# Kernel optimization log

Measured on AMD Instinct MI355X. Metric: run time of the kernel, lower is better.

## Reference

```python
import jax, jax.numpy as jnp
import numpy as np

B, S, D = 4, 2048, 2048
H = 16
Q_LORA = 1536
KV_LORA = 512
D_NOPE = 128
D_ROPE = 64
D_V = 128
MLP = 8192
EPS = 1e-6
THETA = 10000.0


def rmsnorm(x, scale, eps=EPS):
    var = jnp.mean(jnp.square(x.astype(jnp.float32)), axis=-1, keepdims=True)
    return (x * jax.lax.rsqrt(var + eps)).astype(x.dtype) * scale


def rope(x, positions):
    # x: [B, S, H, d], positions: [B, S]
    d = x.shape[-1]
    inv_freq = 1.0 / (THETA ** (jnp.arange(0, d, 2, dtype=jnp.float32) / d))
    ang = positions.astype(jnp.float32)[..., None] * inv_freq  # [B,S,d/2]
    cos = jnp.cos(ang)[:, :, None, :]
    sin = jnp.sin(ang)[:, :, None, :]
    x1, x2 = jnp.split(x, 2, axis=-1)
    return jnp.concatenate([x1 * cos - x2 * sin, x2 * cos + x1 * sin], axis=-1)


def setup_inputs() -> dict:
    key = jax.random.key(0)
    ks = jax.random.split(key, 16)
    sd = lambda fan: 1.0 / np.sqrt(fan)
    inp = {
        'inputs': jax.random.normal(ks[0], (B, S, D), jnp.float32),
        'decoder_segment_ids': jnp.ones((B, S), jnp.int32),
        'decoder_positions': jnp.broadcast_to(jnp.arange(S, dtype=jnp.int32), (B, S)),
        'pre_ln_scale': jnp.ones((D,), jnp.float32),
        'post_ln_scale': jnp.ones((D,), jnp.float32),
        'q_ln_scale': jnp.ones((Q_LORA,), jnp.float32),
        'kv_ln_scale': jnp.ones((KV_LORA,), jnp.float32),
        'wq_a': jax.random.normal(ks[1], (D, Q_LORA), jnp.float32) * sd(D),
        'wq_b': jax.random.normal(ks[2], (Q_LORA, H, D_NOPE + D_ROPE), jnp.float32) * sd(Q_LORA),
        'wkv_a': jax.random.normal(ks[3], (D, KV_LORA + D_ROPE), jnp.float32) * sd(D),
        'wkv_b': jax.random.normal(ks[4], (KV_LORA, H, D_NOPE + D_V), jnp.float32) * sd(KV_LORA),
        'wo_attn': jax.random.normal(ks[5], (H, D_V, D), jnp.float32) * sd(H * D_V),
        'wi_0': jax.random.normal(ks[6], (D, MLP), jnp.float32) * sd(D),
        'wi_1': jax.random.normal(ks[7], (D, MLP), jnp.float32) * sd(D),
        'wo_mlp': jax.random.normal(ks[8], (MLP, D), jnp.float32) * sd(MLP),
    }
    return inp


def reference(inputs, decoder_segment_ids, decoder_positions, pre_ln_scale, post_ln_scale,
              q_ln_scale, kv_ln_scale, wq_a, wq_b, wkv_a, wkv_b, wo_attn, wi_0, wi_1, wo_mlp):
    # ---- pre-norm ----
    lnx = rmsnorm(inputs, pre_ln_scale)

    # ---- MLA attention ----
    # low-rank query: down-proj, norm, up-proj
    q_c = rmsnorm(lnx @ wq_a, q_ln_scale)                       # [B,S,Q_LORA]
    q = jnp.einsum('bsr,rhd->bshd', q_c, wq_b)                  # [B,S,H,nope+rope]
    q_nope, q_rope = q[..., :D_NOPE], q[..., D_NOPE:]

    # compressed kv + decoupled rope key
    kv = lnx @ wkv_a                                            # [B,S,KV_LORA+rope]
    c_kv = rmsnorm(kv[..., :KV_LORA], kv_ln_scale)
    k_rope = kv[..., KV_LORA:][:, :, None, :]                   # [B,S,1,rope]
    kvu = jnp.einsum('bsr,rhd->bshd', c_kv, wkv_b)              # [B,S,H,nope+v]
    k_nope, v = kvu[..., :D_NOPE], kvu[..., D_NOPE:]

    q_rope = rope(q_rope, decoder_positions)
    k_rope = rope(k_rope, decoder_positions)
    k_rope = jnp.broadcast_to(k_rope, (B, S, H, D_ROPE))

    qf = jnp.concatenate([q_nope, q_rope], axis=-1)             # [B,S,H,192]
    kf = jnp.concatenate([k_nope, k_rope], axis=-1)

    scale = 1.0 / np.sqrt(D_NOPE + D_ROPE)
    scores = jnp.einsum('bqhd,bkhd->bhqk', qf, kf) * scale      # [B,H,S,S]

    pos = decoder_positions
    seg = decoder_segment_ids
    mask = (pos[:, :, None] >= pos[:, None, :]) & (seg[:, :, None] == seg[:, None, :])
    scores = jnp.where(mask[:, None, :, :], scores, -1e9)
    probs = jax.nn.softmax(scores, axis=-1)

    attn = jnp.einsum('bhqk,bkhd->bqhd', probs, v)              # [B,S,H,D_V]
    attn_out = jnp.einsum('bqhd,hdm->bqm', attn, wo_attn)       # [B,S,D]

    # ---- residual + post-norm ----
    intermediate = inputs + attn_out
    hidden = rmsnorm(intermediate, post_ln_scale)

    # ---- gated MLP (silu * linear) ----
    mlp = (jax.nn.silu(hidden @ wi_0) * (hidden @ wi_1)) @ wo_mlp

    return mlp + intermediate
```

## Files before the change

### kernel.cpp

```cpp
#include <hip/hip_runtime.h>
#include <stdint.h>

typedef unsigned short u16;
typedef __bf16 bf16x8 __attribute__((ext_vector_type(8)));
typedef float f32x4 __attribute__((ext_vector_type(4)));

#define B_ 4
#define S_ 2048
#define H_ 16
#define TOK (B_*S_)
#define MFMA_B16 __builtin_amdgcn_mfma_f32_16x16x32_bf16
#define LGKM0 asm volatile("s_waitcnt lgkmcnt(0)" ::: "memory")
#define VMC(n) asm volatile("s_waitcnt vmcnt(" #n ")" ::: "memory")
#define SB0 __builtin_amdgcn_sched_barrier(0)

__device__ __forceinline__ u16 f32_bf16(float f) {
    union { float f; unsigned int u; } x; x.f = f;
    return (u16)((x.u + 0x7fffu + ((x.u >> 16) & 1u)) >> 16);
}
__device__ __forceinline__ float bf2f(u16 v) {
    union { unsigned int u; float f; } x; x.u = ((unsigned int)v) << 16; return x.f;
}
__device__ __forceinline__ void gld_lds16(const u16* g, u16* lds) {
    __builtin_amdgcn_global_load_lds(
        (const __attribute__((address_space(1))) unsigned int*)g,
        (__attribute__((address_space(3))) unsigned int*)lds, 16, 0, 0);
}

__global__ void fill_sentinel(float* o, int n) {
    int i = blockIdx.x * 256 + threadIdx.x;
    if (i < n) o[i] = 12345.0f;
}

__global__ __launch_bounds__(256) void transpose_f32_bf16(const float* __restrict__ in, u16* __restrict__ out,
                                                          int K, int N, int Npad) {
    __shared__ float t[32][33];
    int nb = blockIdx.x * 32, kb = blockIdx.y * 32;
    int c = threadIdx.x & 31, r = threadIdx.x >> 5;
#pragma unroll
    for (int i = 0; i < 4; ++i) {
        int kk = kb + r + i * 8, nn = nb + c;
        t[r + i * 8][c] = (kk < K && nn < N) ? in[(size_t)kk * N + nn] : 0.f;
    }
    __syncthreads();
#pragma unroll
    for (int i = 0; i < 4; ++i) {
        int no = nb + r + i * 8, ko = kb + c;
        if (no < Npad && ko < K) out[(size_t)no * K + ko] = f32_bf16(t[c][r + i * 8]);
    }
}

__global__ __launch_bounds__(256) void rmsnorm_f32(const float* __restrict__ in, const float* __restrict__ sc,
                                                   u16* __restrict__ out, int N) {
    int row = blockIdx.x;
    const float* x = in + (size_t)row * N;
    float ss = 0.f;
    for (int c = threadIdx.x * 4; c < N; c += 1024) {
        float4 v = *(const float4*)(x + c);
        ss += v.x * v.x + v.y * v.y + v.z * v.z + v.w * v.w;
    }
#pragma unroll
    for (int off = 32; off; off >>= 1) ss += __shfl_down(ss, off);
    __shared__ float red[4];
    if ((threadIdx.x & 63) == 0) red[threadIdx.x >> 6] = ss;
    __syncthreads();
    float rs = rsqrtf((red[0] + red[1] + red[2] + red[3]) / (float)N + 1e-6f);
    for (int c = threadIdx.x * 4; c < N; c += 1024) {
        float4 v = *(const float4*)(x + c);
        float4 s4 = *(const float4*)(sc + c);
        ushort4 ov;
        ov.x = f32_bf16(v.x * rs * s4.x);
        ov.y = f32_bf16(v.y * rs * s4.y);
        ov.z = f32_bf16(v.z * rs * s4.z);
        ov.w = f32_bf16(v.w * rs * s4.w);
        *(ushort4*)&out[(size_t)row * N + c] = ov;
    }
}

__global__ __launch_bounds__(256) void rmsnorm_bf16(const u16* __restrict__ in, const float* __restrict__ sc,
                                                    u16* __restrict__ out, int N) {
    int row = blockIdx.x;
    const u16* x = in + (size_t)row * N;
    float ss = 0.f;
    for (int c = threadIdx.x * 8; c < N; c += 2048) {
        ushort4 v0 = *(const ushort4*)(x + c);
        ushort4 v1 = *(const ushort4*)(x + c + 4);
        float f0 = bf2f(v0.x), f1 = bf2f(v0.y), f2 = bf2f(v0.z), f3 = bf2f(v0.w);
        float f4 = bf2f(v1.x), f5 = bf2f(v1.y), f6 = bf2f(v1.z), f7 = bf2f(v1.w);
        ss += f0*f0 + f1*f1 + f2*f2 + f3*f3 + f4*f4 + f5*f5 + f6*f6 + f7*f7;
    }
#pragma unroll
    for (int off = 32; off; off >>= 1) ss += __shfl_down(ss, off);
    __shared__ float red[4];
    if ((threadIdx.x & 63) == 0) red[threadIdx.x >> 6] = ss;
    __syncthreads();
    float rs = rsqrtf((red[0] + red[1] + red[2] + red[3]) / (float)N + 1e-6f);
    for (int c = threadIdx.x * 8; c < N; c += 2048) {
        ushort4 v0 = *(const ushort4*)(x + c);
        ushort4 v1 = *(const ushort4*)(x + c + 4);
        ushort4 o0, o1;
        o0.x = f32_bf16(bf2f(v0.x) * rs * sc[c + 0]);
        o0.y = f32_bf16(bf2f(v0.y) * rs * sc[c + 1]);
        o0.z = f32_bf16(bf2f(v0.z) * rs * sc[c + 2]);
        o0.w = f32_bf16(bf2f(v0.w) * rs * sc[c + 3]);
        o1.x = f32_bf16(bf2f(v1.x) * rs * sc[c + 4]);
        o1.y = f32_bf16(bf2f(v1.y) * rs * sc[c + 5]);
        o1.z = f32_bf16(bf2f(v1.z) * rs * sc[c + 6]);
        o1.w = f32_bf16(bf2f(v1.w) * rs * sc[c + 7]);
        *(ushort4*)&out[(size_t)row * N + c] = o0;
        *(ushort4*)&out[(size_t)row * N + c + 4] = o1;
    }
}

__global__ __launch_bounds__(128) void kv_post(const u16* __restrict__ kv, const float* __restrict__ scale,
                                               const int* __restrict__ pos, u16* __restrict__ ckv,
                                               u16* __restrict__ kr) {
    int row = blockIdx.x;
    const u16* x = kv + (size_t)row * 640;
    int c = threadIdx.x * 4;
    ushort4 v = *(const ushort4*)(x + c);
    float f0 = bf2f(v.x), f1 = bf2f(v.y), f2 = bf2f(v.z), f3 = bf2f(v.w);
    float ss = f0*f0 + f1*f1 + f2*f2 + f3*f3;
#pragma unroll
    for (int off = 32; off; off >>= 1) ss += __shfl_down(ss, off);
    __shared__ float red[2];
    if ((threadIdx.x & 63) == 0) red[threadIdx.x >> 6] = ss;
    __syncthreads();
    float rs = rsqrtf((red[0] + red[1]) * (1.f / 512.f) + 1e-6f);
    float4 s4 = *(const float4*)(scale + c);
    ushort4 ov;
    ov.x = f32_bf16(f0 * rs * s4.x);
    ov.y = f32_bf16(f1 * rs * s4.y);
    ov.z = f32_bf16(f2 * rs * s4.z);
    ov.w = f32_bf16(f3 * rs * s4.w);
    *(ushort4*)&ckv[(size_t)row * 512 + c] = ov;
    if (threadIdx.x < 32) {
        int i = threadIdx.x;
        float x1 = bf2f(x[512 + i]), x2 = bf2f(x[544 + i]);
        float inv = expf(-(float)(2 * i) * (1.f / 64.f) * 9.2103403719761836f);
        float ang = (float)pos[row] * inv;
        float sn, cs; sincosf(ang, &sn, &cs);
        kr[(size_t)row * 64 + i]      = f32_bf16(x1 * cs - x2 * sn);
        kr[(size_t)row * 64 + 32 + i] = f32_bf16(x2 * cs + x1 * sn);
    }
}

__global__ __launch_bounds__(64) void q_rope_inplace(u16* __restrict__ q, const int* __restrict__ pos) {
    int token = blockIdx.x, h = blockIdx.y;
    u16* p = q + ((size_t)token * 16 + h) * 192;
    int t = threadIdx.x, i = t & 31;
    float x1 = bf2f(p[128 + i]), x2 = bf2f(p[160 + i]);
    float inv = expf(-(float)(2 * i) * (1.f / 64.f) * 9.2103403719761836f);
    float ang = (float)pos[token] * inv;
    float sn, cs; sincosf(ang, &sn, &cs);
    float val = (t < 32) ? (x1 * cs - x2 * sn) : (x2 * cs + x1 * sn);
    p[128 + t] = f32_bf16(val);
}

__global__ __launch_bounds__(320) void kv_build(const u16* __restrict__ kvu, const u16* __restrict__ kr,
                                                u16* __restrict__ kf, u16* __restrict__ vf, int tok0) {
    int local = blockIdx.x, h = blockIdx.y;
    int token = tok0 + local;
    int b = token >> 11, s = token & 2047;
    int bh = b * 16 + h;
    int tile = s >> 6, ki = s & 63;
    const u16* u = kvu + ((size_t)local * 16 + h) * 256;
    int t = threadIdx.x;
    if (t < 192) {
        u16 val = (t < 128) ? u[t] : kr[(size_t)token * 64 + (t - 128)];
        int byte = (ki * 384 + t * 2) ^ ((ki & 7) << 4);
        kf[(size_t)bh * (S_ * 192) + (size_t)tile * 12288 + (byte >> 1)] = val;
    } else {
        int dv = t - 192;
        u16 val = u[128 + dv];
        int byte = (dv * 128 + ki * 2) ^ ((dv & 7) << 4);
        vf[(size_t)bh * (S_ * 128) + (size_t)tile * 8192 + (byte >> 1)] = val;
    }
}

__global__ __launch_bounds__(256) void gemm128(const u16* __restrict__ A, const u16* __restrict__ Bt,
                                               u16* __restrict__ C, int M, int N, int K) {
    __shared__ u16 As[128 * 32];
    __shared__ u16 Bs[128 * 32];
    const int l = threadIdx.x & 63, w = threadIdx.x >> 6;
    const int wr = w >> 1, wc = w & 1;
    const int m0 = blockIdx.y * 128, n0 = blockIdx.x * 128;
    const int lm = l & 15, lg = l >> 4;
    const int srow = l >> 2, sk = (l & 3) * 8;
    f32x4 acc[4][4] = {};
    for (int k0 = 0; k0 < K; k0 += 32) {
#pragma unroll
        for (int i = 0; i < 2; ++i) {
            int c = w * 2 + i;
            gld_lds16(A  + (size_t)(m0 + c * 16 + srow) * K + k0 + sk, &As[c * 512]);
            gld_lds16(Bt + (size_t)(n0 + c * 16 + srow) * K + k0 + sk, &Bs[c * 512]);
        }
        __syncthreads();
        bf16x8 a[4], b[4];
#pragma unroll
        for (int m = 0; m < 4; ++m) a[m] = *(const bf16x8*)&As[(wr * 64 + m * 16 + lm) * 32 + lg * 8];
#pragma unroll
        for (int n = 0; n < 4; ++n) b[n] = *(const bf16x8*)&Bs[(wc * 64 + n * 16 + lm) * 32 + lg * 8];
#pragma unroll
        for (int m = 0; m < 4; ++m)
#pragma unroll
            for (int n = 0; n < 4; ++n)
                acc[m][n] = MFMA_B16(a[m], b[n], acc[m][n], 0, 0, 0);
        __syncthreads();
    }
#pragma unroll
    for (int m = 0; m < 4; ++m)
#pragma unroll
        for (int j = 0; j < 4; ++j) {
            int row = m0 + wr * 64 + m * 16 + lg * 4 + j;
            size_t base = (size_t)row * N + n0 + wc * 64;
#pragma unroll
            for (int n = 0; n < 4; ++n)
                C[base + n * 16 + lm] = f32_bf16(acc[m][n][j]);
        }
}

template<int EPI>
__global__ __launch_bounds__(512, 1) void gemm256(const u16* __restrict__ A, const u16* __restrict__ Bt,
                                                  void* __restrict__ Cv, const void* __restrict__ Rv,
                                                  int M, int N, int K) {
    __shared__ u16 lds[65536];
    char* ldsb = (char*)lds;
    const int tid = threadIdx.x;
    const int l = tid & 63, w = tid >> 6;
    const int wr = w >> 2, wcn = w & 3;
    const int lm = l & 15, lg = l >> 4;
    const int m0 = blockIdx.y * 256, n0 = blockIdx.x * 256;

    int sr[2], scb[2];
#pragma unroll
    for (int ld = 0; ld < 2; ++ld) {
        int P = tid * 16 + ld * 8192;
        sr[ld] = P >> 7;
        scb[ld] = (P & 127) ^ ((sr[ld] & 7) << 4);
    }
    const u16* Ab = A + (size_t)m0 * K;
    const u16* Bb = Bt + (size_t)n0 * K;

    f32x4 acc[8][4] = {};

    auto stageU = [&](int unit, int tt) {
#pragma unroll
        for (int ld = 0; ld < 2; ++ld) {
            int r = sr[ld];
            const u16* src;
            if (unit == 0)      src = Ab + (size_t)((r >> 6) * 128 + (r & 63)) * K + tt * 64 + (scb[ld] >> 1);
            else if (unit == 1) src = Ab + (size_t)((r >> 6) * 128 + 64 + (r & 63)) * K + tt * 64 + (scb[ld] >> 1);
            else if (unit == 2) src = Bb + (size_t)((r >> 5) * 64 + (r & 31)) * K + tt * 64 + (scb[ld] >> 1);
            else                src = Bb + (size_t)((r >> 5) * 64 + 32 + (r & 31)) * K + tt * 64 + (scb[ld] >> 1);
            gld_lds16(src, (u16*)(ldsb + (tt & 1) * 65536 + unit * 16384 + tid * 16 + ld * 8192));
        }
    };
    auto readA = [&](int buf, int fm, int ks) -> bf16x8 {
        int lr = wr * 64 + (fm & 3) * 16 + lm;
        int byte = lr * 128 + ((ks * 64 + lg * 16) ^ ((lr & 7) << 4));
        return *(const bf16x8*)(ldsb + buf * 65536 + (fm >> 2) * 16384 + byte);
    };
    auto readB = [&](int buf, int fn, int ks) -> bf16x8 {
        int lr = wcn * 32 + (fn & 1) * 16 + lm;
        int byte = lr * 128 + ((ks * 64 + lg * 16) ^ ((lr & 7) << 4));
        return *(const bf16x8*)(ldsb + buf * 65536 + (2 + (fn >> 1)) * 16384 + byte);
    };

    const int nt = K >> 6;
    stageU(0, 0); stageU(2, 0); stageU(3, 0); stageU(1, 0);
    VMC(2);
    __builtin_amdgcn_s_barrier();

#pragma unroll 1
    for (int t = 0; t < nt; ++t) {
        const int buf = t & 1;
        const bool nx = (t + 1 < nt);
        bf16x8 a0, a1, a2, a3, a4, a5, a6, a7;
        bf16x8 b0 = readB(buf, 0, 0), b1 = readB(buf, 0, 1), b2 = readB(buf, 1, 0), b3 = readB(buf, 1, 1);
        a0 = readA(buf, 0, 0); a1 = readA(buf, 0, 1); a2 = readA(buf, 1, 0); a3 = readA(buf, 1, 1);
        a4 = readA(buf, 2, 0); a5 = readA(buf, 2, 1); a6 = readA(buf, 3, 0); a7 = readA(buf, 3, 1);
        if (nx) stageU(0, t + 1);
        __builtin_amdgcn_s_barrier();
        LGKM0;
        SB0;
        __builtin_amdgcn_s_setprio(1);
        acc[0][0] = MFMA_B16(a0, b0, acc[0][0], 0, 0, 0);
        acc[0][0] = MFMA_B16(a1, b1, acc[0][0], 0, 0, 0);
        acc[0][1] = MFMA_B16(a0, b2, acc[0][1], 0, 0, 0);
        acc[0][1] = MFMA_B16(a1, b3, acc[0][1], 0, 0, 0);
        acc[1][0] = MFMA_B16(a2, b0, acc[1][0], 0, 0, 0);
        acc[1][0] = MFMA_B16(a3, b1, acc[1][0], 0, 0, 0);
        acc[1][1] = MFMA_B16(a2, b2, acc[1][1], 0, 0, 0);
        acc[1][1] = MFMA_B16(a3, b3, acc[1][1], 0, 0, 0);
        acc[2][0] = MFMA_B16(a4, b0, acc[2][0], 0, 0, 0);
        acc[2][0] = MFMA_B16(a5, b1, acc[2][0], 0, 0, 0);
        acc[2][1] = MFMA_B16(a4, b2, acc[2][1], 0, 0, 0);
        acc[2][1] = MFMA_B16(a5, b3, acc[2][1], 0, 0, 0);
        acc[3][0] = MFMA_B16(a6, b0, acc[3][0], 0, 0, 0);
        acc[3][0] = MFMA_B16(a7, b1, acc[3][0], 0, 0, 0);
        acc[3][1] = MFMA_B16(a6, b2, acc[3][1], 0, 0, 0);
        acc[3][1] = MFMA_B16(a7, b3, acc[3][1], 0, 0, 0);
        __builtin_amdgcn_s_setprio(0);
        __builtin_amdgcn_s_barrier();
        bf16x8 c0 = readB(buf, 2, 0), c1 = readB(buf, 2, 1), c2 = readB(buf, 3, 0), c3 = readB(buf, 3, 1);
        if (nx) { stageU(2, t + 1); VMC(4); } else { VMC(0); }
        __builtin_amdgcn_s_barrier();
        LGKM0;
        SB0;
        __builtin_amdgcn_s_setprio(1);
        acc[0][2] = MFMA_B16(a0, c0, acc[0][2], 0, 0, 0);
        acc[0][2] = MFMA_B16(a1, c1, acc[0][2], 0, 0, 0);
        acc[0][3] = MFMA_B16(a0, c2, acc[0][3], 0, 0, 0);
        acc[0][3] = MFMA_B16(a1, c3, acc[0][3], 0, 0, 0);
        acc[1][2] = MFMA_B16(a2, c0, acc[1][2], 0, 0, 0);
        acc[1][2] = MFMA_B16(a3, c1, acc[1][2], 0, 0, 0);
        acc[1][3] = MFMA_B16(a2, c2, acc[1][3], 0, 0, 0);
        acc[1][3] = MFMA_B16(a3, c3, acc[1][3], 0, 0, 0);
        acc[2][2] = MFMA_B16(a4, c0, acc[2][2], 0, 0, 0);
        acc[2][2] = MFMA_B16(a5, c1, acc[2][2], 0, 0, 0);
        acc[2][3] = MFMA_B16(a4, c2, acc[2][3], 0, 0, 0);
        acc[2][3] = MFMA_B16(a5, c3, acc[2][3], 0, 0, 0);
        acc[3][2] = MFMA_B16(a6, c0, acc[3][2], 0, 0, 0);
        acc[3][2] = MFMA_B16(a7, c1, acc[3][2], 0, 0, 0);
        acc[3][3] = MFMA_B16(a6, c2, acc[3][3], 0, 0, 0);
        acc[3][3] = MFMA_B16(a7, c3, acc[3][3], 0, 0, 0);
        __builtin_amdgcn_s_setprio(0);
        __builtin_amdgcn_s_barrier();
        a0 = readA(buf, 4, 0); a1 = readA(buf, 4, 1); a2 = readA(buf, 5, 0); a3 = readA(buf, 5, 1);
        a4 = readA(buf, 6, 0); a5 = readA(buf, 6, 1); a6 = readA(buf, 7, 0); a7 = readA(buf, 7, 1);
        if (nx) stageU(3, t + 1);
        __builtin_amdgcn_s_barrier();
        LGKM0;
        SB0;
        __builtin_amdgcn_s_setprio(1);
        acc[4][2] = MFMA_B16(a0, c0, acc[4][2], 0, 0, 0);
        acc[4][2] = MFMA_B16(a1, c1, acc[4][2], 0, 0, 0);
        acc[4][3] = MFMA_B16(a0, c2, acc[4][3], 0, 0, 0);
        acc[4][3] = MFMA_B16(a1, c3, acc[4][3], 0, 0, 0);
        acc[5][2] = MFMA_B16(a2, c0, acc[5][2], 0, 0, 0);
        acc[5][2] = MFMA_B16(a3, c1, acc[5][2], 0, 0, 0);
        acc[5][3] = MFMA_B16(a2, c2, acc[5][3], 0, 0, 0);
        acc[5][3] = MFMA_B16(a3, c3, acc[5][3], 0, 0, 0);
        acc[6][2] = MFMA_B16(a4, c0, acc[6][2], 0, 0, 0);
        acc[6][2] = MFMA_B16(a5, c1, acc[6][2], 0, 0, 0);
        acc[6][3] = MFMA_B16(a4, c2, acc[6][3], 0, 0, 0);
        acc[6][3] = MFMA_B16(a5, c3, acc[6][3], 0, 0, 0);
        acc[7][2] = MFMA_B16(a6, c0, acc[7][2], 0, 0, 0);
        acc[7][2] = MFMA_B16(a7, c1, acc[7][2], 0, 0, 0);
        acc[7][3] = MFMA_B16(a6, c2, acc[7][3], 0, 0, 0);
        acc[7][3] = MFMA_B16(a7, c3, acc[7][3], 0, 0, 0);
        __builtin_amdgcn_s_setprio(0);
        __builtin_amdgcn_s_barrier();
        if (nx) { stageU(1, t + 1); VMC(2); }
        __builtin_amdgcn_s_barrier();
        SB0;
        __builtin_amdgcn_s_setprio(1);
        acc[4][0] = MFMA_B16(a0, b0, acc[4][0], 0, 0, 0);
        acc[4][0] = MFMA_B16(a1, b1, acc[4][0], 0, 0, 0);
        acc[4][1] = MFMA_B16(a0, b2, acc[4][1], 0, 0, 0);
        acc[4][1] = MFMA_B16(a1, b3, acc[4][1], 0, 0, 0);
        acc[5][0] = MFMA_B16(a2, b0, acc[5][0], 0, 0, 0);
        acc[5][0] = MFMA_B16(a3, b1, acc[5][0], 0, 0, 0);
        acc[5][1] = MFMA_B16(a2, b2, acc[5][1], 0, 0, 0);
        acc[5][1] = MFMA_B16(a3, b3, acc[5][1], 0, 0, 0);
        acc[6][0] = MFMA_B16(a4, b0, acc[6][0], 0, 0, 0);
        acc[6][0] = MFMA_B16(a5, b1, acc[6][0], 0, 0, 0);
        acc[6][1] = MFMA_B16(a4, b2, acc[6][1], 0, 0, 0);
        acc[6][1] = MFMA_B16(a5, b3, acc[6][1], 0, 0, 0);
        acc[7][0] = MFMA_B16(a6, b0, acc[7][0], 0, 0, 0);
        acc[7][0] = MFMA_B16(a7, b1, acc[7][0], 0, 0, 0);
        acc[7][1] = MFMA_B16(a6, b2, acc[7][1], 0, 0, 0);
        acc[7][1] = MFMA_B16(a7, b3, acc[7][1], 0, 0, 0);
        __builtin_amdgcn_s_setprio(0);
        __builtin_amdgcn_s_barrier();
    }
#pragma unroll
    for (int fm = 0; fm < 8; ++fm)
#pragma unroll
        for (int j = 0; j < 4; ++j) {
            int row = m0 + wr * 128 + fm * 16 + lg * 4 + j;
            size_t base = (size_t)row * N + n0 + wcn * 64;
#pragma unroll
            for (int fn = 0; fn < 4; ++fn) {
                size_t idx = base + fn * 16 + lm;
                float v = acc[fm][fn][j];
                if (EPI == 0) {
                    ((u16*)Cv)[idx] = f32_bf16(v);
                } else if (EPI == 1) {
                    ((float*)Cv)[idx] = v + ((const float*)Rv)[idx];
                } else {
                    float x0 = bf2f(((const u16*)Rv)[idx]);
                    float sl = x0 / (1.f + expf(-x0));
                    ((u16*)Cv)[idx] = f32_bf16(sl * v);
                }
            }
        }
}

__global__ __launch_bounds__(256, 3) void attn_fwd(const u16* __restrict__ qf, const u16* __restrict__ kfs,
                                                   const u16* __restrict__ vfs, u16* __restrict__ attn) {
    __shared__ u16 Ks[64 * 192];
    __shared__ u16 Vs[128 * 64];
    __shared__ u16 Ps[4][1024];
    const int lin = blockIdx.y * gridDim.x + blockIdx.x;
    const int xcd = lin & 7, j = lin >> 3;
    const int bh = xcd * 8 + (j >> 4);
    const int px = j & 15;
    const int b = bh >> 4, h = bh & 15;
    const int l = threadIdx.x & 63, w = threadIdx.x >> 6;
    const int lm = l & 15, g = l >> 4;
    const u16* kb0 = kfs + (size_t)bh * (S_ * 192);
    const u16* vb0 = vfs + (size_t)bh * (S_ * 128);
    const float scale = 0.07216878364870322f;

    auto stageK = [&](int kt2) {
        const u16* kc = kb0 + (size_t)kt2 * 12288;
#pragma unroll
        for (int i = 0; i < 6; ++i) {
            int c = w + i * 4;
            gld_lds16(kc + c * 512 + l * 8, &Ks[c * 512]);
        }
    };
    auto stageV = [&](int kt2) {
        const u16* vc = vb0 + (size_t)kt2 * 8192;
#pragma unroll
        for (int i = 0; i < 4; ++i) {
            int c = w + i * 4;
            gld_lds16(vc + c * 512 + l * 8, &Vs[c * 512]);
        }
    };

    stageK(0);

    for (int pass = 0; pass < 2; ++pass) {
        const int qb = pass ? (31 - px) : px;
        const int qrow = qb * 64 + w * 16 + lm;
        const u16* qp = qf + (((size_t)(b * S_ + qrow)) * 16 + h) * 192 + g * 8;
        bf16x8 qr[6];
#pragma unroll
        for (int c = 0; c < 6; ++c) qr[c] = *(const bf16x8*)(qp + c * 32);
        f32x4 o[8] = {};
        float mrow[4] = {-1e30f, -1e30f, -1e30f, -1e30f};
        float lrow[4] = {0.f, 0.f, 0.f, 0.f};
        for (int kt = 0; kt <= qb; ++kt) {
            __syncthreads();
            stageV(kt);
            f32x4 sc[4] = {};
#pragma unroll
            for (int nf = 0; nf < 4; ++nf) {
                int key = nf * 16 + lm;
                int kswz = (key & 7) << 4;
#pragma unroll
                for (int c = 0; c < 6; ++c) {
                    int byte = (key * 384 + (c * 32 + g * 8) * 2) ^ kswz;
                    bf16x8 kv = *(const bf16x8*)((const char*)Ks + byte);
                    sc[nf] = MFMA_B16(qr[c], kv, sc[nf], 0, 0, 0);
                }
            }
            LGKM0;
            __builtin_amdgcn_s_barrier();
            if (kt < qb) stageK(kt + 1);
#pragma unroll
            for (int jj = 0; jj < 4; ++jj) {
                const int q_g = qb * 64 + w * 16 + g * 4 + jj;
                float mx = -1e30f;
#pragma unroll
                for (int nf = 0; nf < 4; ++nf) {
                    int key_g = kt * 64 + nf * 16 + lm;
                    float v = sc[nf][jj] * scale;
                    v = (key_g > q_g) ? -1e30f : v;
                    sc[nf][jj] = v;
                    mx = fmaxf(mx, v);
                }
                mx = fmaxf(mx, __shfl_xor(mx, 1));
                mx = fmaxf(mx, __shfl_xor(mx, 2));
                mx = fmaxf(mx, __shfl_xor(mx, 4));
                mx = fmaxf(mx, __shfl_xor(mx, 8));
                float newm = fmaxf(mrow[jj], mx);
                float fac = __expf(mrow[jj] - newm);
                mrow[jj] = newm;
                float rs = 0.f;
                u16 pb[4];
#pragma unroll
                for (int nf = 0; nf < 4; ++nf) {
                    float pv = __expf(sc[nf][jj] - newm);
                    rs += pv;
                    pb[nf] = f32_bf16(pv);
                }
                rs += __shfl_xor(rs, 1);
                rs += __shfl_xor(rs, 2);
                rs += __shfl_xor(rs, 4);
                rs += __shfl_xor(rs, 8);
                lrow[jj] = lrow[jj] * fac + rs;
#pragma unroll
                for (int n = 0; n < 8; ++n) o[n][jj] *= fac;
                int row = g * 4 + jj;
                int rswz = (row & 7) << 4;
#pragma unroll
                for (int nf = 0; nf < 4; ++nf) {
                    int byte = (row * 128 + (nf * 16 + lm) * 2) ^ rswz;
                    *(u16*)((char*)&Ps[w][0] + byte) = pb[nf];
                }
            }
            if (kt < qb) { VMC(6); } else { VMC(0); }
            __builtin_amdgcn_s_barrier();
            SB0;
#pragma unroll
            for (int kc2 = 0; kc2 < 2; ++kc2) {
                int pbyte = (lm * 128 + (kc2 * 32 + g * 8) * 2) ^ ((lm & 7) << 4);
                bf16x8 pa = *(const bf16x8*)((const char*)&Ps[w][0] + pbyte);
#pragma unroll
                for (int n = 0; n < 8; ++n) {
                    int dv = n * 16 + lm;
                    int vbyte = (dv * 128 + (kc2 * 32 + g * 8) * 2) ^ ((dv & 7) << 4);
                    bf16x8 vv = *(const bf16x8*)((const char*)Vs + vbyte);
                    o[n] = MFMA_B16(pa, vv, o[n], 0, 0, 0);
                }
            }
        }
#pragma unroll
        for (int jj = 0; jj < 4; ++jj) {
            float inv = 1.f / lrow[jj];
            int s = qb * 64 + w * 16 + g * 4 + jj;
            size_t base = ((size_t)(b * S_ + s)) * (H_ * 128) + h * 128;
#pragma unroll
            for (int n = 0; n < 8; ++n)
                attn[base + n * 16 + lm] = f32_bf16(o[n][jj] * inv);
        }
        if (pass == 0) stageK(0);
    }
}

extern "C" void kernel_launch(void* const* d_in, const int* in_sizes, int n_in,
                              void* d_out, int out_size, void* d_ws, size_t ws_size,
                              hipStream_t stream) {
    (void)in_sizes; (void)n_in;
    const float* inputs = (const float*)d_in[0];
    const int*   pos    = (const int*)d_in[2];
    const float* pre_s  = (const float*)d_in[3];
    const float* post_s = (const float*)d_in[4];
    const float* q_s    = (const float*)d_in[5];
    const float* kv_s   = (const float*)d_in[6];
    const float* wq_a   = (const float*)d_in[7];
    const float* wq_b   = (const float*)d_in[8];
    const float* wkv_a  = (const float*)d_in[9];
    const float* wkv_b  = (const float*)d_in[10];
    const float* wo_at  = (const float*)d_in[11];
    const float* wi0    = (const float*)d_in[12];
    const float* wi1    = (const float*)d_in[13];
    const float* wom    = (const float*)d_in[14];
    float* out = (float*)d_out;

    char* p = (char*)d_ws;
    auto alloc = [&](size_t n) { char* r = p; p += (n + 255) & ~(size_t)255; return r; };
    char* R1   = alloc((size_t)134217728);
    u16* vf    = (u16*)alloc((size_t)33554432);
    u16* aslot = (u16*)alloc((size_t)33554432);
    u16* wslot = (u16*)alloc((size_t)33554432);
    u16* ckv   = (u16*)alloc((size_t)8388608);
    u16* krope = (u16*)alloc((size_t)1048576);
    if ((size_t)(p - (char*)d_ws) > ws_size) {
        fill_sentinel<<<(out_size + 255) / 256, 256, 0, stream>>>(out, out_size);
        return;
    }
    u16* kf    = (u16*)R1;
    u16* q_c   = (u16*)R1;
    u16* kvtmp = (u16*)(R1 + 25165824);
    u16* q     = (u16*)(R1 + 50331648);
    u16* lnx   = (u16*)(R1 + 100663296);
    u16* kvu   = (u16*)(R1 + 100663296);
    u16* X     = (u16*)R1;

    rmsnorm_f32<<<TOK, 256, 0, stream>>>(inputs, pre_s, lnx, 2048);
    transpose_f32_bf16<<<dim3(48, 64), 256, 0, stream>>>(wq_a, wslot, 2048, 1536, 1536);
    gemm256<0><<<dim3(6, 32), 512, 0, stream>>>(lnx, wslot, q_c, nullptr, TOK, 1536, 2048);
    rmsnorm_bf16<<<TOK, 256, 0, stream>>>(q_c, q_s, q_c, 1536);
    transpose_f32_bf16<<<dim3(20, 64), 256, 0, stream>>>(wkv_a, wslot, 2048, 576, 640);
    gemm128<<<dim3(5, 64), 256, 0, stream>>>(lnx, wslot, kvtmp, TOK, 640, 2048);
    kv_post<<<TOK, 128, 0, stream>>>(kvtmp, kv_s, pos, ckv, krope);
    transpose_f32_bf16<<<dim3(96, 48), 256, 0, stream>>>(wq_b, wslot, 1536, 3072, 3072);
    gemm256<0><<<dim3(12, 32), 512, 0, stream>>>(q_c, wslot, q, nullptr, TOK, 3072, 1536);
    q_rope_inplace<<<dim3(TOK, 16), 64, 0, stream>>>(q, pos);
    transpose_f32_bf16<<<dim3(128, 16), 256, 0, stream>>>(wkv_b, wslot, 512, 4096, 4096);
    for (int ch = 0; ch < 2; ++ch) {
        int t0 = ch * 4096;
        gemm256<0><<<dim3(16, 16), 512, 0, stream>>>(ckv + (size_t)t0 * 512, wslot, kvu, nullptr, 4096, 4096, 512);
        kv_build<<<dim3(4096, 16), 320, 0, stream>>>(kvu, krope, kf, vf, t0);
    }
    attn_fwd<<<dim3(16, 64), 256, 0, stream>>>(q, kf, vf, aslot);
    transpose_f32_bf16<<<dim3(64, 64), 256, 0, stream>>>(wo_at, wslot, 2048, 2048, 2048);
    gemm256<1><<<dim3(8, 32), 512, 0, stream>>>(aslot, wslot, out, inputs, TOK, 2048, 2048);
    rmsnorm_f32<<<TOK, 256, 0, stream>>>(out, post_s, aslot, 2048);
    transpose_f32_bf16<<<dim3(256, 64), 256, 0, stream>>>(wi0, wslot, 2048, 8192, 8192);
    gemm256<0><<<dim3(32, 32), 512, 0, stream>>>(aslot, wslot, X, nullptr, TOK, 8192, 2048);
    transpose_f32_bf16<<<dim3(256, 64), 256, 0, stream>>>(wi1, wslot, 2048, 8192, 8192);
    gemm256<2><<<dim3(32, 32), 512, 0, stream>>>(aslot, wslot, X, X, TOK, 8192, 2048);
    transpose_f32_bf16<<<dim3(64, 256), 256, 0, stream>>>(wom, wslot, 8192, 2048, 2048);
    gemm256<1><<<dim3(8, 32), 512, 0, stream>>>(X, wslot, out, out, TOK, 2048, 8192);
}
```

Baseline: 1.669 ms.

## Software-pipeline LDS fragment reads across GEMM k-iterations with split A registers

Restructures the GEMM main loop so the first half of the A fragments and the second-half B fragments for the next k-tile are read from LDS during the current iteration, using separate low/high A register sets. Partial lgkmcnt waits replace full LDS drains, and the staging order of the global-to-LDS loads is changed to match. The aim is to hide LDS read latency behind MFMA work and cut pipeline bubbles between phases. The cost is higher register pressure and subtle wait-count correctness that depends on the exact load ordering.

New measurement: 1.671 ms. About the same (+0.1%).

```diff
diff --git a/kernel.cpp b/kernel.cpp
--- a/kernel.cpp
+++ b/kernel.cpp
@@ -11,6 +11,7 @@
 #define TOK (B_*S_)
 #define MFMA_B16 __builtin_amdgcn_mfma_f32_16x16x32_bf16
 #define LGKM0 asm volatile("s_waitcnt lgkmcnt(0)" ::: "memory")
+#define LGKM(n) asm volatile("s_waitcnt lgkmcnt(" #n ")" ::: "memory")
 #define VMC(n) asm volatile("s_waitcnt vmcnt(" #n ")" ::: "memory")
 #define SB0 __builtin_amdgcn_sched_barrier(0)
 
@@ -268,110 +269,122 @@
     };
 
     const int nt = K >> 6;
-    stageU(0, 0); stageU(2, 0); stageU(3, 0); stageU(1, 0);
-    VMC(2);
+    bf16x8 b0, b1, b2, b3, c0, c1, c2, c3;
+    bf16x8 al0, al1, al2, al3, al4, al5, al6, al7;
+    bf16x8 ah0, ah1, ah2, ah3, ah4, ah5, ah6, ah7;
+
+    stageU(0, 0); stageU(3, 0); stageU(2, 0); stageU(1, 0);
+    VMC(4);
     __builtin_amdgcn_s_barrier();
+    al0 = readA(0, 0, 0); al1 = readA(0, 0, 1); al2 = readA(0, 1, 0); al3 = readA(0, 1, 1);
+    al4 = readA(0, 2, 0); al5 = readA(0, 2, 1); al6 = readA(0, 3, 0); al7 = readA(0, 3, 1);
+    c0 = readB(0, 2, 0); c1 = readB(0, 2, 1); c2 = readB(0, 3, 0); c3 = readB(0, 3, 1);
 
 #pragma unroll 1
     for (int t = 0; t < nt; ++t) {
         const int buf = t & 1;
         const bool nx = (t + 1 < nt);
-        bf16x8 a0, a1, a2, a3, a4, a5, a6, a7;
-        bf16x8 b0 = readB(buf, 0, 0), b1 = readB(buf, 0, 1), b2 = readB(buf, 1, 0), b3 = readB(buf, 1, 1);
-        a0 = readA(buf, 0, 0); a1 = readA(buf, 0, 1); a2 = readA(buf, 1, 0); a3 = readA(buf, 1, 1);
-        a4 = readA(buf, 2, 0); a5 = readA(buf, 2, 1); a6 = readA(buf, 3, 0); a7 = readA(buf, 3, 1);
-        if (nx) stageU(0, t + 1);
-        __builtin_amdgcn_s_barrier();
-        LGKM0;
+        if (nx) { stageU(0, t + 1); VMC(2); } else { VMC(0); }
+        __builtin_amdgcn_s_barrier();
+        b0 = readB(buf, 0, 0); b1 = readB(buf, 0, 1); b2 = readB(buf, 1, 0); b3 = readB(buf, 1, 1);
+        ah0 = readA(buf, 4, 0); ah1 = readA(buf, 4, 1); ah2 = readA(buf, 5, 0); ah3 = readA(buf, 5, 1);
+        ah4 = readA(buf, 6, 0); ah5 = readA(buf, 6, 1); ah6 = readA(buf, 7, 0); ah7 = readA(buf, 7, 1);
+        LGKM(8);
         SB0;
         __builtin_amdgcn_s_setprio(1);
-        acc[0][0] = MFMA_B16(a0, b0, acc[0][0], 0, 0, 0);
-        acc[0][0] = MFMA_B16(a1, b1, acc[0][0], 0, 0, 0);
-        acc[0][1] = MFMA_B16(a0, b2, acc[0][1], 0, 0, 0);
-        acc[0][1] = MFMA_B16(a1, b3, acc[0][1], 0, 0, 0);
-        acc[1][0] = MFMA_B16(a2, b0, acc[1][0], 0, 0, 0);
-        acc[1][0] = MFMA_B16(a3, b1, acc[1][0], 0, 0, 0);
-        acc[1][1] = MFMA_B16(a2, b2, acc[1][1], 0, 0, 0);
-        acc[1][1] = MFMA_B16(a3, b3, acc[1][1], 0, 0, 0);
-        acc[2][0] = MFMA_B16(a4, b0, acc[2][0], 0, 0, 0);
-        acc[2][0] = MFMA_B16(a5, b1, acc[2][0], 0, 0, 0);
-        acc[2][1] = MFMA_B16(a4, b2, acc[2][1], 0, 0, 0);
-        acc[2][1] = MFMA_B16(a5, b3, acc[2][1], 0, 0, 0);
-        acc[3][0] = MFMA_B16(a6, b0, acc[3][0], 0, 0, 0);
-        acc[3][0] = MFMA_B16(a7, b1, acc[3][0], 0, 0, 0);
-        acc[3][1] = MFMA_B16(a6, b2, acc[3][1], 0, 0, 0);
-        acc[3][1] = MFMA_B16(a7, b3, acc[3][1], 0, 0, 0);
+        acc[0][0] = MFMA_B16(al0, b0, acc[0][0], 0, 0, 0);
+        acc[0][0] = MFMA_B16(al1, b1, acc[0][0], 0, 0, 0);
+        acc[0][1] = MFMA_B16(al0, b2, acc[0][1], 0, 0, 0);
+        acc[0][1] = MFMA_B16(al1, b3, acc[0][1], 0, 0, 0);
+        acc[1][0] = MFMA_B16(al2, b0, acc[1][0], 0, 0, 0);
+        acc[1][0] = MFMA_B16(al3, b1, acc[1][0], 0, 0, 0);
+        acc[1][1] = MFMA_B16(al2, b2, acc[1][1], 0, 0, 0);
+        acc[1][1] = MFMA_B16(al3, b3, acc[1][1], 0, 0, 0);
+        acc[2][0] = MFMA_B16(al4, b0, acc[2][0], 0, 0, 0);
+        acc[2][0] = MFMA_B16(al5, b1, acc[2][0], 0, 0, 0);
+        acc[2][1] = MFMA_B16(al4, b2, acc[2][1], 0, 0, 0);
+        acc[2][1] = MFMA_B16(al5, b3, acc[2][1], 0, 0, 0);
+        acc[3][0] = MFMA_B16(al6, b0, acc[3][0], 0, 0, 0);
+        acc[3][0] = MFMA_B16(al7, b1, acc[3][0], 0, 0, 0);
+        acc[3][1] = MFMA_B16(al6, b2, acc[3][1], 0, 0, 0);
+        acc[3][1] = MFMA_B16(al7, b3, acc[3][1], 0, 0, 0);
         __builtin_amdgcn_s_setprio(0);
         __builtin_amdgcn_s_barrier();
-        bf16x8 c0 = readB(buf, 2, 0), c1 = readB(buf, 2, 1), c2 = readB(buf, 3, 0), c3 = readB(buf, 3, 1);
-        if (nx) { stageU(2, t + 1); VMC(4); } else { VMC(0); }
-        __builtin_amdgcn_s_barrier();
-        LGKM0;
+        if (nx) stageU(3, t + 1);
+        __builtin_amdgcn_s_barrier();
+        __builtin_amdgcn_s_setprio(1);
+        acc[0][2] = MFMA_B16(al0, c0, acc[0][2], 0, 0, 0);
+        acc[0][2] = MFMA_B16(al1, c1, acc[0][2], 0, 0, 0);
+        acc[0][3] = MFMA_B16(al0, c2, acc[0][3], 0, 0, 0);
+        acc[0][3] = MFMA_B16(al1, c3, acc[0][3], 0, 0, 0);
+        acc[1][2] = MFMA_B16(al2, c0, acc[1][2], 0, 0, 0);
+        acc[1][2] = MFMA_B16(al3, c1, acc[1][2], 0, 0, 0);
+        acc[1][3] = MFMA_B16(al2, c2, acc[1][3], 0, 0, 0);
+        acc[1][3] = MFMA_B16(al3, c3, acc[1][3], 0, 0, 0);
+        acc[2][2] = MFMA_B16(al4, c0, acc[2][2], 0, 0, 0);
+        acc[2][2] = MFMA_B16(al5, c1, acc[2][2], 0, 0, 0);
+        acc[2][3] = MFMA_B16(al4, c2, acc[2][3], 0, 0, 0);
+        acc[2][3] = MFMA_B16(al5, c3, acc[2][3], 0, 0, 0);
+        acc[3][2] = MFMA_B16(al6, c0, acc[3][2], 0, 0, 0);
+        acc[3][2] = MFMA_B16(al7, c1, acc[3][2], 0, 0, 0);
+        acc[3][3] = MFMA_B16(al6, c2, acc[3][3], 0, 0, 0);
+        acc[3][3] = MFMA_B16(al7, c3, acc[3][3], 0, 0, 0);
+        __builtin_amdgcn_s_setprio(0);
+        __builtin_amdgcn_s_barrier();
+        if (nx) {
+            stageU(2, t + 1); stageU(1, t + 1);
+            VMC(6);
+        }
+        __builtin_amdgcn_s_barrier();
+        if (nx) {
+            al0 = readA(buf ^ 1, 0, 0); al1 = readA(buf ^ 1, 0, 1); al2 = readA(buf ^ 1, 1, 0); al3 = readA(buf ^ 1, 1, 1);
+            al4 = readA(buf ^ 1, 2, 0); al5 = readA(buf ^ 1, 2, 1); al6 = readA(buf ^ 1, 3, 0); al7 = readA(buf ^ 1, 3, 1);
+            LGKM(8);
+        } else {
+            LGKM0;
+        }
         SB0;
         __builtin_amdgcn_s_setprio(1);
-        acc[0][2] = MFMA_B16(a0, c0, acc[0][2], 0, 0, 0);
-        acc[0][2] = MFMA_B16(a1, c1, acc[0][2], 0, 0, 0);
-        acc[0][3] = MFMA_B16(a0, c2, acc[0][3], 0, 0, 0);
-        acc[0][3] = MFMA_B16(a1, c3, acc[0][3], 0, 0, 0);
-        acc[1][2] = MFMA_B16(a2, c0, acc[1][2], 0, 0, 0);
-        acc[1][2] = MFMA_B16(a3, c1, acc[1][2], 0, 0, 0);
-        acc[1][3] = MFMA_B16(a2, c2, acc[1][3], 0, 0, 0);
-        acc[1][3] = MFMA_B16(a3, c3, acc[1][3], 0, 0, 0);
-        acc[2][2] = MFMA_B16(a4, c0, acc[2][2], 0, 0, 0);
-        acc[2][2] = MFMA_B16(a5, c1, acc[2][2], 0, 0, 0);
-        acc[2][3] = MFMA_B16(a4, c2, acc[2][3], 0, 0, 0);
-        acc[2][3] = MFMA_B16(a5, c3, acc[2][3], 0, 0, 0);
-        acc[3][2] = MFMA_B16(a6, c0, acc[3][2], 0, 0, 0);
-        acc[3][2] = MFMA_B16(a7, c1, acc[3][2], 0, 0, 0);
-        acc[3][3] = MFMA_B16(a6, c2, acc[3][3], 0, 0, 0);
-        acc[3][3] = MFMA_B16(a7, c3, acc[3][3], 0, 0, 0);
+        acc[4][2] = MFMA_B16(ah0, c0, acc[4][2], 0, 0, 0);
+        acc[4][2] = MFMA_B16(ah1, c1, acc[4][2], 0, 0, 0);
+        acc[4][3] = MFMA_B16(ah0, c2, acc[4][3], 0, 0, 0);
+        acc[4][3] = MFMA_B16(ah1, c3, acc[4][3], 0, 0, 0);
+        acc[5][2] = MFMA_B16(ah2, c0, acc[5][2], 0, 0, 0);
+        acc[5][2] = MFMA_B16(ah3, c1, acc[5][2], 0, 0, 0);
+        acc[5][3] = MFMA_B16(ah2, c2, acc[5][3], 0, 0, 0);
+        acc[5][3] = MFMA_B16(ah3, c3, acc[5][3], 0, 0, 0);
+        acc[6][2] = MFMA_B16(ah4, c0, acc[6][2], 0, 0, 0);
+        acc[6][2] = MFMA_B16(ah5, c1, acc[6][2], 0, 0, 0);
+        acc[6][3] = MFMA_B16(ah4, c2, acc[6][3], 0, 0, 0);
+        acc[6][3] = MFMA_B16(ah5, c3, acc[6][3], 0, 0, 0);
+        acc[7][2] = MFMA_B16(ah6, c0, acc[7][2], 0, 0, 0);
+        acc[7][2] = MFMA_B16(ah7, c1, acc[7][2], 0, 0, 0);
+        acc[7][3] = MFMA_B16(ah6, c2, acc[7][3], 0, 0, 0);
+        acc[7][3] = MFMA_B16(ah7, c3, acc[7][3], 0, 0, 0);
         __builtin_amdgcn_s_setprio(0);
         __builtin_amdgcn_s_barrier();
-        a0 = readA(buf, 4, 0); a1 = readA(buf, 4, 1); a2 = readA(buf, 5, 0); a3 = readA(buf, 5, 1);
-        a4 = readA(buf, 6, 0); a5 = readA(buf, 6, 1); a6 = readA(buf, 7, 0); a7 = readA(buf, 7, 1);
-        if (nx) stageU(3, t + 1);
-        __builtin_amdgcn_s_barrier();
-        LGKM0;
-        SB0;
+        if (nx) VMC(4);
+        __builtin_amdgcn_s_barrier();
+        if (nx) {
+            c0 = readB(buf ^ 1, 2, 0); c1 = readB(buf ^ 1, 2, 1); c2 = readB(buf ^ 1, 3, 0); c3 = readB(buf ^ 1, 3, 1);
+        }
         __builtin_amdgcn_s_setprio(1);
-        acc[4][2] = MFMA_B16(a0, c0, acc[4][2], 0, 0, 0);
-        acc[4][2] = MFMA_B16(a1, c1, acc[4][2], 0, 0, 0);
-        acc[4][3] = MFMA_B16(a0, c2, acc[4][3], 0, 0, 0);
-        acc[4][3] = MFMA_B16(a1, c3, acc[4][3], 0, 0, 0);
-        acc[5][2] = MFMA_B16(a2, c0, acc[5][2], 0, 0, 0);
-        acc[5][2] = MFMA_B16(a3, c1, acc[5][2], 0, 0, 0);
-        acc[5][3] = MFMA_B16(a2, c2, acc[5][3], 0, 0, 0);
-        acc[5][3] = MFMA_B16(a3, c3, acc[5][3], 0, 0, 0);
-        acc[6][2] = MFMA_B16(a4, c0, acc[6][2], 0, 0, 0);
-        acc[6][2] = MFMA_B16(a5, c1, acc[6][2], 0, 0, 0);
-        acc[6][3] = MFMA_B16(a4, c2, acc[6][3], 0, 0, 0);
-        acc[6][3] = MFMA_B16(a5, c3, acc[6][3], 0, 0, 0);
-        acc[7][2] = MFMA_B16(a6, c0, acc[7][2], 0, 0, 0);
-        acc[7][2] = MFMA_B16(a7, c1, acc[7][2], 0, 0, 0);
-        acc[7][3] = MFMA_B16(a6, c2, acc[7][3], 0, 0, 0);
-        acc[7][3] = MFMA_B16(a7, c3, acc[7][3], 0, 0, 0);
-        __builtin_amdgcn_s_setprio(0);
-        __builtin_amdgcn_s_barrier();
-        if (nx) { stageU(1, t + 1); VMC(2); }
-        __builtin_amdgcn_s_barrier();
-        SB0;
-        __builtin_amdgcn_s_setprio(1);
-        acc[4][0] = MFMA_B16(a0, b0, acc[4][0], 0, 0, 0);
-        acc[4][0] = MFMA_B16(a1, b1, acc[4][0], 0, 0, 0);
-        acc[4][1] = MFMA_B16(a0, b2, acc[4][1], 0, 0, 0);
-        acc[4][1] = MFMA_B16(a1, b3, acc[4][1], 0, 0, 0);
-        acc[5][0] = MFMA_B16(a2, b0, acc[5][0], 0, 0, 0);
-        acc[5][0] = MFMA_B16(a3, b1, acc[5][0], 0, 0, 0);
-        acc[5][1] = MFMA_B16(a2, b2, acc[5][1], 0, 0, 0);
-        acc[5][1] = MFMA_B16(a3, b3, acc[5][1], 0, 0, 0);
-        acc[6][0] = MFMA_B16(a4, b0, acc[6][0], 0, 0, 0);
-        acc[6][0] = MFMA_B16(a5, b1, acc[6][0], 0, 0, 0);
-        acc[6][1] = MFMA_B16(a4, b2, acc[6][1], 0, 0, 0);
-        acc[6][1] = MFMA_B16(a5, b3, acc[6][1], 0, 0, 0);
-        acc[7][0] = MFMA_B16(a6, b0, acc[7][0], 0, 0, 0);
-        acc[7][0] = MFMA_B16(a7, b1, acc[7][0], 0, 0, 0);
-        acc[7][1] = MFMA_B16(a6, b2, acc[7][1], 0, 0, 0);
-        acc[7][1] = MFMA_B16(a7, b3, acc[7][1], 0, 0, 0);
+        acc[4][0] = MFMA_B16(ah0, b0, acc[4][0], 0, 0, 0);
+        acc[4][0] = MFMA_B16(ah1, b1, acc[4][0], 0, 0, 0);
+        acc[4][1] = MFMA_B16(ah0, b2, acc[4][1], 0, 0, 0);
+        acc[4][1] = MFMA_B16(ah1, b3, acc[4][1], 0, 0, 0);
+        acc[5][0] = MFMA_B16(ah2, b0, acc[5][0], 0, 0, 0);
+        acc[5][0] = MFMA_B16(ah3, b1, acc[5][0], 0, 0, 0);
+        acc[5][1] = MFMA_B16(ah2, b2, acc[5][1], 0, 0, 0);
+        acc[5][1] = MFMA_B16(ah3, b3, acc[5][1], 0, 0, 0);
+        acc[6][0] = MFMA_B16(ah4, b0, acc[6][0], 0, 0, 0);
+        acc[6][0] = MFMA_B16(ah5, b1, acc[6][0], 0, 0, 0);
+        acc[6][1] = MFMA_B16(ah4, b2, acc[6][1], 0, 0, 0);
+        acc[6][1] = MFMA_B16(ah5, b3, acc[6][1], 0, 0, 0);
+        acc[7][0] = MFMA_B16(ah6, b0, acc[7][0], 0, 0, 0);
+        acc[7][0] = MFMA_B16(ah7, b1, acc[7][0], 0, 0, 0);
+        acc[7][1] = MFMA_B16(ah6, b2, acc[7][1], 0, 0, 0);
+        acc[7][1] = MFMA_B16(ah7, b3, acc[7][1], 0, 0, 0);
         __builtin_amdgcn_s_setprio(0);
         __builtin_amdgcn_s_barrier();
     }
```
